# Kernel tuning notes

Measured on AMD Instinct MI355X. Metric: run time of the kernel, lower is better.

The kernel has to match this reference:

```python
import jax, jax.numpy as jnp
import numpy as np

N = 100000      # nodes (categories_nums[0])
E = 1600000     # edges
FEAT = 16       # features_num
HID = 32        # hidden
IDE = 16        # id_embed_size
EMB = 8         # embed_size
CAT_MAX = 1000  # categorical vocab (categories_nums[1:])
K = 3           # TAGConv hops (sparse=False)
NC = 2          # num_class
IN_DIM = IDE + 2 * EMB + HID  # 64 -> TAGConv input
EPS = 1e-5


def layer_norm(x, g, b):
    m = jnp.mean(x, axis=-1, keepdims=True)
    v = jnp.mean((x - m) ** 2, axis=-1, keepdims=True)
    return (x - m) * jax.lax.rsqrt(v + EPS) * g + b


def setup_inputs() -> dict:
    key = jax.random.key(0)
    ks = jax.random.split(key, 20)
    s = 0.05
    return {
        "x": jax.random.normal(ks[0], (N, FEAT), jnp.float32),
        "edge_index": jax.random.randint(ks[1], (2, E), 0, N, jnp.int64),
        "edge_weight": jax.random.uniform(ks[2], (E,), jnp.float32),
        "categories_value": jax.random.randint(ks[3], (N, 3), 0, CAT_MAX, jnp.int64),
        "id_table": jax.random.normal(ks[4], (N, IDE), jnp.float32) * s,
        "lin0_id_W": jax.random.normal(ks[5], (IDE, IDE), jnp.float32) * s,
        "lin0_id_b": jnp.zeros((IDE,), jnp.float32),
        "emb1": jax.random.normal(ks[6], (CAT_MAX, EMB), jnp.float32) * s,
        "emb2": jax.random.normal(ks[7], (CAT_MAX, EMB), jnp.float32) * s,
        "lin0_emb_W": jax.random.normal(ks[8], (2 * EMB, 2 * EMB), jnp.float32) * s,
        "lin0_emb_b": jnp.zeros((2 * EMB,), jnp.float32),
        "lin0_W": jax.random.normal(ks[9], (FEAT, HID), jnp.float32) * s,
        "lin0_b": jnp.zeros((HID,), jnp.float32),
        "ln0_g": jnp.ones((IN_DIM,), jnp.float32),
        "ln0_b": jnp.zeros((IN_DIM,), jnp.float32),
        "tag_W": jax.random.normal(ks[10], (K + 1, IN_DIM, HID), jnp.float32) * s,
        "tag_b": jnp.zeros((HID,), jnp.float32),
        "ln1_g": jnp.ones((HID,), jnp.float32),
        "ln1_b": jnp.zeros((HID,), jnp.float32),
        "lin1_W": jax.random.normal(ks[11], (HID, NC), jnp.float32) * s,
        "lin1_b": jnp.zeros((NC,), jnp.float32),
    }


def reference(x, edge_index, edge_weight, categories_value, id_table, lin0_id_W,
              lin0_id_b, emb1, emb2, lin0_emb_W, lin0_emb_b, lin0_W, lin0_b,
              ln0_g, ln0_b, tag_W, tag_b, ln1_g, ln1_b, lin1_W, lin1_b):
    # eval mode: dropouts are identity
    h = jax.nn.elu(x @ lin0_W + lin0_b)                       # [N, HID]
    ide = id_table[categories_value[:, 0]]                    # [N, IDE]
    ide = jax.nn.elu(ide @ lin0_id_W + lin0_id_b)
    er = jnp.concatenate([emb1[categories_value[:, 1]],
                          emb2[categories_value[:, 2]]], axis=1)  # [N, 2*EMB]
    er = jax.nn.elu(er @ lin0_emb_W + lin0_emb_b)
    feat = jnp.concatenate([ide, h, er], axis=1)              # [N, IN_DIM]
    feat = layer_norm(feat, ln0_g, ln0_b)

    # TAGConv: gcn_norm without self-loops, K-hop propagation
    row, col = edge_index[0], edge_index[1]                   # source -> target
    deg = jax.ops.segment_sum(edge_weight, col, num_segments=N)
    dis = jnp.where(deg > 0, deg ** -0.5, 0.0)
    norm = dis[row] * edge_weight * dis[col]                  # [E]

    out = feat @ tag_W[0]                                     # [N, HID]
    xk = feat
    for k in range(1, K + 1):
        xk = jax.ops.segment_sum(xk[row] * norm[:, None], col, num_segments=N)
        out = out + xk @ tag_W[k]
    out = out + tag_b

    out = jax.nn.relu(out)
    out = layer_norm(out, ln1_g, ln1_b)
    out = out @ lin1_W + lin1_b                               # [N, NC]
    return jax.nn.log_softmax(out, axis=-1)
```

## Files before the change

### kernel.cpp

```cpp
#include <hip/hip_runtime.h>
#include <hip/hip_bf16.h>

typedef unsigned short u16;
typedef unsigned int   u32;
typedef unsigned long long u64;
typedef u32 u32x2 __attribute__((ext_vector_type(2)));
typedef u32 u32x4 __attribute__((ext_vector_type(4)));

#define FIX_SCALE 16777216.0f
#define FIX_INV   (1.0f / 16777216.0f)
#define CNT_SHIFT 40
#define DEG_MASK  ((1ULL << CNT_SHIFT) - 1)

__device__ __forceinline__ float b2f(u16 u) { return __uint_as_float(((u32)u) << 16); }
__device__ __forceinline__ u16 f2b(float f) {
    u32 u = __float_as_uint(f);
    return (u16)((u + 0x7FFFu + ((u >> 16) & 1u)) >> 16);
}
__device__ __forceinline__ float elu(float v) { return v > 0.f ? v : expm1f(v); }
__device__ __forceinline__ float ldf(const void* p, size_t i, int f32) {
    return f32 ? ((const float*)p)[i] : b2f(((const u16*)p)[i]);
}
__device__ __forceinline__ float plo(u32 a) { return __uint_as_float(a << 16); }
__device__ __forceinline__ float phi(u32 a) { return __uint_as_float(a & 0xFFFF0000u); }

__global__ void k_flags(const u32* __restrict__ gw, const int* __restrict__ ei,
                        const int* __restrict__ cat, int* __restrict__ flags) {
    if (threadIdx.x == 0 && blockIdx.x == 0) {
        flags[0] = (gw[0] == 0x3F800000u) ? 1 : 0;
        flags[1] = ((ei[1]  | ei[3]  | ei[5]  | ei[7])  == 0) ? 2 : 1;
        flags[2] = ((cat[1] | cat[3] | cat[5] | cat[7]) == 0) ? 2 : 1;
    }
}

__global__ __launch_bounds__(256) void k_feathist(
    const void* __restrict__ x, const int* __restrict__ cat,
    const void* __restrict__ id_table, const void* __restrict__ W_id, const void* __restrict__ b_id,
    const void* __restrict__ emb1, const void* __restrict__ emb2,
    const void* __restrict__ W_emb, const void* __restrict__ b_emb,
    const void* __restrict__ W0, const void* __restrict__ b0,
    const void* __restrict__ g0, const void* __restrict__ bb0,
    u32* __restrict__ feat,
    const int* __restrict__ ei, const void* __restrict__ ew,
    u64* __restrict__ packed, u16* __restrict__ rank,
    const int* __restrict__ flags, int N, int E, int nbN)
{
    __shared__ float sW0[512];
    __shared__ float sb0[32];
    __shared__ float sWid[256];
    __shared__ float sbid[16];
    __shared__ float sWe[256];
    __shared__ float sbe[16];
    __shared__ float sg[64], sb[64];
    int tid = threadIdx.x;
    int f32 = flags[0], s = flags[1], cs = flags[2];

    int e0 = blockIdx.x * 512 + tid;
    int e1 = e0 + 256;
    u64 old0 = 0, old1 = 0;
    bool h0 = (e0 < E), h1 = (e1 < E);
    const int* colp = ei + (size_t)E * s;
    if (h0) {
        int cdst = colp[(size_t)e0 * s];
        float w = ldf(ew, e0, f32);
        old0 = atomicAdd(&packed[cdst], (1ULL << CNT_SHIFT) | (u64)(w * FIX_SCALE + 0.5f));
    }
    if (h1) {
        int cdst = colp[(size_t)e1 * s];
        float w = ldf(ew, e1, f32);
        old1 = atomicAdd(&packed[cdst], (1ULL << CNT_SHIFT) | (u64)(w * FIX_SCALE + 0.5f));
    }

    if (blockIdx.x < nbN) {
        for (int i = tid; i < 512; i += 256) sW0[i] = ldf(W0, i, f32);
        if (tid < 32) sb0[tid] = ldf(b0, tid, f32);
        sWid[tid] = ldf(W_id, tid, f32);
        if (tid < 16) sbid[tid] = ldf(b_id, tid, f32);
        sWe[tid] = ldf(W_emb, tid, f32);
        if (tid < 16) sbe[tid] = ldf(b_emb, tid, f32);
        if (tid < 64) { sg[tid] = ldf(g0, tid, f32); sb[tid] = ldf(bb0, tid, f32); }
        __syncthreads();

        int i = blockIdx.x * 256 + tid;
        if (i < N) {
            size_t cb = (size_t)i * 3 * cs;
            int c0 = cat[cb], c1 = cat[cb + cs], c2 = cat[cb + 2 * cs];
            float f[64];
            {
                float t[16];
                #pragma unroll
                for (int q = 0; q < 16; q++) t[q] = ldf(id_table, (size_t)c0 * 16 + q, f32);
                #pragma unroll
                for (int j = 0; j < 16; j++) {
                    float a = sbid[j];
                    #pragma unroll
                    for (int ff = 0; ff < 16; ff++) a += t[ff] * sWid[ff * 16 + j];
                    f[j] = elu(a);
                }
            }
            {
                float t[16];
                #pragma unroll
                for (int q = 0; q < 16; q++) t[q] = ldf(x, (size_t)i * 16 + q, f32);
                #pragma unroll
                for (int j = 0; j < 32; j++) {
                    float a = sb0[j];
                    #pragma unroll
                    for (int ff = 0; ff < 16; ff++) a += t[ff] * sW0[ff * 32 + j];
                    f[16 + j] = elu(a);
                }
            }
            {
                float t[16];
                #pragma unroll
                for (int q = 0; q < 8; q++) t[q] = ldf(emb1, (size_t)c1 * 8 + q, f32);
                #pragma unroll
                for (int q = 0; q < 8; q++) t[8 + q] = ldf(emb2, (size_t)c2 * 8 + q, f32);
                #pragma unroll
                for (int j = 0; j < 16; j++) {
                    float a = sbe[j];
                    #pragma unroll
                    for (int ff = 0; ff < 16; ff++) a += t[ff] * sWe[ff * 16 + j];
                    f[48 + j] = elu(a);
                }
            }
            float m = 0.f;
            #pragma unroll
            for (int d = 0; d < 64; d++) m += f[d];
            m *= (1.f / 64.f);
            float var = 0.f;
            #pragma unroll
            for (int d = 0; d < 64; d++) { float df = f[d] - m; var += df * df; }
            var *= (1.f / 64.f);
            float rs = rsqrtf(var + 1e-5f);
            #pragma unroll
            for (int d = 0; d < 64; d++) f[d] = (f[d] - m) * rs * sg[d] + sb[d];

            u32* fp = feat + (size_t)i * 32;
            #pragma unroll
            for (int q = 0; q < 32; q++) fp[q] = ((u32)f2b(f[2 * q + 1]) << 16) | f2b(f[2 * q]);
        }
    }
    if (h0) rank[e0] = (u16)(old0 >> CNT_SHIFT);
    if (h1) rank[e1] = (u16)(old1 >> CNT_SHIFT);
}

__global__ __launch_bounds__(256) void k_zproj(
    const u32* __restrict__ feat, const void* __restrict__ tagW,
    float* __restrict__ oacc, u32* __restrict__ z1, u32* __restrict__ z2, u32* __restrict__ z3,
    const int* __restrict__ flags, int N)
{
    __shared__ float sT[4 * 2056];
    int tid = threadIdx.x;
    int f32 = flags[0];
    for (int i = tid; i < 8192; i += 256) {
        int k = i >> 11, r = i & 2047;
        sT[k * 2056 + r] = ldf(tagW, i, f32);
    }
    __syncthreads();

    int nblk = blockIdx.x * 32 + (tid >> 3);
    if (nblk >= N) return;
    int sub = tid & 7, kk = sub >> 1, h = sub & 1;

    const u32x4* fp4 = (const u32x4*)(feat + (size_t)nblk * 32);
    float f[64];
    #pragma unroll
    for (int q = 0; q < 8; q++) {
        u32x4 a = fp4[q];
        f[8 * q + 0] = plo(a.x); f[8 * q + 1] = phi(a.x);
        f[8 * q + 2] = plo(a.y); f[8 * q + 3] = phi(a.y);
        f[8 * q + 4] = plo(a.z); f[8 * q + 5] = phi(a.z);
        f[8 * q + 6] = plo(a.w); f[8 * q + 7] = phi(a.w);
    }

    float o[16];
    #pragma unroll
    for (int j = 0; j < 16; j++) o[j] = 0.f;
    const float* T = sT + kk * 2056 + h * 16;
    #pragma unroll 4
    for (int d = 0; d < 64; d++) {
        float fd = f[d];
        #pragma unroll
        for (int j = 0; j < 16; j++) o[j] += fd * T[d * 32 + j];
    }

    if (kk == 0) {
        float4* op = (float4*)(oacc + (size_t)nblk * 32 + h * 16);
        #pragma unroll
        for (int q = 0; q < 4; q++) op[q] = make_float4(o[4 * q], o[4 * q + 1], o[4 * q + 2], o[4 * q + 3]);
    } else {
        u32* zp = ((kk == 1) ? z1 : (kk == 2) ? z2 : z3) + (size_t)nblk * 16 + h * 8;
        #pragma unroll
        for (int jj = 0; jj < 8; jj++) zp[jj] = ((u32)f2b(o[2 * jj + 1]) << 16) | f2b(o[2 * jj]);
    }
}

__global__ __launch_bounds__(256) void k_scan1(const u64* __restrict__ packed, int* __restrict__ ebuf,
                                               int* __restrict__ bsum, float* __restrict__ dis, int N)
{
    __shared__ int sdat[256];
    int tid = threadIdx.x;
    int i = blockIdx.x * 256 + tid;
    u64 pv = (i < N) ? packed[i] : 0ULL;
    int v = (int)(pv >> CNT_SHIFT);
    sdat[tid] = v;
    __syncthreads();
    for (int off = 1; off < 256; off <<= 1) {
        int t = (tid >= off) ? sdat[tid - off] : 0;
        __syncthreads();
        sdat[tid] += t;
        __syncthreads();
    }
    if (i < N) {
        ebuf[i] = sdat[tid] - v;
        u64 db = pv & DEG_MASK;
        dis[i] = db ? rsqrtf((float)db * FIX_INV) : 0.f;
    }
    if (tid == 255) bsum[blockIdx.x] = sdat[255];
}

__global__ __launch_bounds__(512) void k_scan2(const int* __restrict__ bsum, int* __restrict__ boff, int NB)
{
    __shared__ int sdat[512];
    __shared__ int scarry;
    int tid = threadIdx.x;
    if (tid == 0) scarry = 0;
    __syncthreads();
    for (int base = 0; base < NB; base += 512) {
        int i = base + tid;
        int v = (i < NB) ? bsum[i] : 0;
        sdat[tid] = v;
        __syncthreads();
        for (int off = 1; off < 512; off <<= 1) {
            int t = (tid >= off) ? sdat[tid - off] : 0;
            __syncthreads();
            sdat[tid] += t;
            __syncthreads();
        }
        if (i < NB) boff[i] = scarry + sdat[tid] - v;
        __syncthreads();
        if (tid == 0) scarry += sdat[511];
        __syncthreads();
    }
}

__global__ __launch_bounds__(256) void k_scan3(const int* __restrict__ ebuf, const int* __restrict__ boff,
                                               int* __restrict__ rowptr, int N, int E)
{
    int i = blockIdx.x * 256 + threadIdx.x;
    if (i >= N) return;
    rowptr[i] = boff[blockIdx.x] + ebuf[i];
    if (i == N - 1) rowptr[N] = E;
}

__global__ __launch_bounds__(256) void k_scatter(const int* __restrict__ ei, const void* __restrict__ ew,
                                                 const float* __restrict__ dis, const u16* __restrict__ rank,
                                                 const int* __restrict__ rowptr, int2* __restrict__ csr,
                                                 const int* __restrict__ flags, int E)
{
    int f32 = flags[0], s = flags[1];
    const int* row = ei;
    const int* col = ei + (size_t)E * s;
    int e = blockIdx.x * 256 + threadIdx.x;
    if (e >= E) return;
    int r = row[(size_t)e * s], c = col[(size_t)e * s];
    float nrm = dis[r] * ldf(ew, e, f32) * dis[c];
    csr[rowptr[c] + (int)rank[e]] = make_int2(r, __float_as_int(nrm));
}

template<int ADD>
__global__ __launch_bounds__(256) void k_ahop(
    const u32* __restrict__ zin, const u32* __restrict__ zadd, u32* __restrict__ uout,
    const int* __restrict__ rowptr, const int2* __restrict__ csr, int N)
{
    int tid = threadIdx.x;
    int node = blockIdx.x * 4 + (tid >> 6);
    if (node >= N) return;
    int lane = tid & 63;
    int o = (lane >> 3) & 7;
    int c = lane & 7;
    int start = rowptr[node], end = rowptr[node + 1];

    const u32x2* fin2 = (const u32x2*)zin;
    float v0 = 0.f, v1 = 0.f, v2 = 0.f, v3 = 0.f;
    int e = start;
    for (; e + 16 <= end; e += 16) {
        int2 ma = csr[e + o];
        int2 mb = csr[e + 8 + o];
        u32x2 aa = fin2[(size_t)(u32)ma.x * 8 + c];
        u32x2 ab = fin2[(size_t)(u32)mb.x * 8 + c];
        float wa = __int_as_float(ma.y), wb = __int_as_float(mb.y);
        v0 += plo(aa.x) * wa; v1 += phi(aa.x) * wa; v2 += plo(aa.y) * wa; v3 += phi(aa.y) * wa;
        v0 += plo(ab.x) * wb; v1 += phi(ab.x) * wb; v2 += plo(ab.y) * wb; v3 += phi(ab.y) * wb;
    }
    for (; e < end; e += 8) {
        int ee = e + o;
        int2 m = (ee < end) ? csr[ee] : make_int2(0, 0);
        u32x2 a = fin2[(size_t)(u32)m.x * 8 + c];
        float w = __int_as_float(m.y);
        v0 += plo(a.x) * w; v1 += phi(a.x) * w; v2 += plo(a.y) * w; v3 += phi(a.y) * w;
    }
    v0 += __shfl_xor(v0, 8);  v1 += __shfl_xor(v1, 8);  v2 += __shfl_xor(v2, 8);  v3 += __shfl_xor(v3, 8);
    v0 += __shfl_xor(v0, 16); v1 += __shfl_xor(v1, 16); v2 += __shfl_xor(v2, 16); v3 += __shfl_xor(v3, 16);
    v0 += __shfl_xor(v0, 32); v1 += __shfl_xor(v1, 32); v2 += __shfl_xor(v2, 32); v3 += __shfl_xor(v3, 32);

    if (lane < 8) {
        if (ADD) {
            u32x2 z = ((const u32x2*)zadd)[(size_t)node * 8 + lane];
            v0 += plo(z.x); v1 += phi(z.x); v2 += plo(z.y); v3 += phi(z.y);
        }
        u32x2 pw;
        pw.x = ((u32)f2b(v1) << 16) | f2b(v0);
        pw.y = ((u32)f2b(v3) << 16) | f2b(v2);
        ((u32x2*)uout)[(size_t)node * 8 + lane] = pw;
    }
}

__global__ __launch_bounds__(256) void k_head(
    const float* __restrict__ oacc, const u32* __restrict__ t1,
    const void* __restrict__ tag_b,
    const void* __restrict__ g1, const void* __restrict__ b1,
    const void* __restrict__ W1, const void* __restrict__ bb1,
    void* __restrict__ out, const int* __restrict__ flags, int N)
{
    __shared__ float stb[32], sg[32], sbb[32], sW1[64], sb1v[2];
    int tid = threadIdx.x;
    int f32 = flags[0];
    if (tid < 32) { stb[tid] = ldf(tag_b, tid, f32); sg[tid] = ldf(g1, tid, f32); sbb[tid] = ldf(b1, tid, f32); }
    if (tid < 64) sW1[tid] = ldf(W1, tid, f32);
    if (tid < 2) sb1v[tid] = ldf(bb1, tid, f32);
    __syncthreads();

    int i = blockIdx.x * 256 + tid;
    if (i >= N) return;

    float acc[32];
    const float4* oa4 = (const float4*)(oacc + (size_t)i * 32);
    #pragma unroll
    for (int q = 0; q < 8; q++) {
        float4 t = oa4[q];
        acc[4 * q] = t.x; acc[4 * q + 1] = t.y; acc[4 * q + 2] = t.z; acc[4 * q + 3] = t.w;
    }
    const u32x2* tp = (const u32x2*)t1 + (size_t)i * 8;
    #pragma unroll
    for (int q = 0; q < 8; q++) {
        u32x2 z = tp[q];
        acc[4 * q]     += plo(z.x); acc[4 * q + 1] += phi(z.x);
        acc[4 * q + 2] += plo(z.y); acc[4 * q + 3] += phi(z.y);
    }
    float o[32]; float m = 0.f;
    #pragma unroll
    for (int j = 0; j < 32; j++) { float t = acc[j] + stb[j]; t = t > 0.f ? t : 0.f; o[j] = t; m += t; }
    m *= (1.f / 32.f);
    float var = 0.f;
    #pragma unroll
    for (int j = 0; j < 32; j++) { float d = o[j] - m; var += d * d; }
    var *= (1.f / 32.f);
    float rs = rsqrtf(var + 1e-5f);
    float z0 = sb1v[0], z1 = sb1v[1];
    #pragma unroll
    for (int j = 0; j < 32; j++) {
        float t = (o[j] - m) * rs * sg[j] + sbb[j];
        z0 += t * sW1[2 * j];
        z1 += t * sW1[2 * j + 1];
    }
    float mx = fmaxf(z0, z1);
    float l = mx + logf(expf(z0 - mx) + expf(z1 - mx));
    if (f32) {
        ((float*)out)[(size_t)i * 2]     = z0 - l;
        ((float*)out)[(size_t)i * 2 + 1] = z1 - l;
    } else {
        *((u32*)((u16*)out + (size_t)i * 2)) = ((u32)f2b(z1 - l) << 16) | f2b(z0 - l);
    }
}

extern "C" void kernel_launch(void* const* d_in, const int* in_sizes, int n_in,
                              void* d_out, int out_size, void* d_ws, size_t ws_size,
                              hipStream_t stream)
{
    const void* x        = d_in[0];
    const int*  ei       = (const int*)d_in[1];
    const void* ew       = d_in[2];
    const int*  cat      = (const int*)d_in[3];
    const void* id_table = d_in[4];
    const void* W_id     = d_in[5];
    const void* b_id     = d_in[6];
    const void* emb1     = d_in[7];
    const void* emb2     = d_in[8];
    const void* W_emb    = d_in[9];
    const void* b_emb    = d_in[10];
    const void* W0       = d_in[11];
    const void* b0       = d_in[12];
    const void* g0       = d_in[13];
    const void* bb0      = d_in[14];
    const void* tagW     = d_in[15];
    const void* tag_b    = d_in[16];
    const void* g1       = d_in[17];
    const void* b1       = d_in[18];
    const void* W1       = d_in[19];
    const void* bb1      = d_in[20];

    int N = in_sizes[0] / 16;
    int E = in_sizes[2];
    int nb = (N + 255) / 256;
    int eb = (E + 255) / 256;
    int eb2 = (E + 511) / 512;
    int zb = (N + 31) / 32;

    char* ws = (char*)d_ws;
    size_t off = 0;
    int*   flags  = (int*)(ws + off);   off += 256;
    float* oacc   = (float*)(ws + off); off += (size_t)N * 32 * 4;
    u32*   feat   = (u32*)(ws + off);   off += (size_t)N * 32 * 4;
    u32*   z1     = (u32*)(ws + off);   off += (size_t)N * 16 * 4;
    u32*   z2     = (u32*)(ws + off);   off += (size_t)N * 16 * 4;
    u32*   z3     = (u32*)(ws + off);   off += (size_t)N * 16 * 4;
    u32*   u2     = (u32*)(ws + off);   off += (size_t)N * 16 * 4;
    int2*  csr    = (int2*)(ws + off);  off += (size_t)E * 8;
    int*   rowptr = (int*)(ws + off);   off += ((size_t)N + 1) * 4;
    off = (off + 255) & ~(size_t)255;
    u16*   rank   = (u16*)(ws + off);   off += (size_t)E * 2;
    off = (off + 255) & ~(size_t)255;
    u64*   packed = (u64*)(ws + off);   off += (size_t)N * 8;
    int*   ebuf   = (int*)(ws + off);   off += (size_t)N * 4;
    float* dis    = (float*)(ws + off); off += (size_t)N * 4;
    int*   bsum   = (int*)(ws + off);   off += (size_t)nb * 4;
    int*   boff   = (int*)(ws + off);   off += (size_t)nb * 4;

    hipMemsetAsync(packed, 0, (size_t)N * 8, stream);
    k_flags<<<1, 64, 0, stream>>>((const u32*)g0, ei, cat, flags);

    k_feathist<<<eb2, 256, 0, stream>>>(x, cat, id_table, W_id, b_id, emb1, emb2, W_emb, b_emb,
                                        W0, b0, g0, bb0, feat,
                                        ei, ew, packed, rank, flags, N, E, nb);
    k_zproj<<<zb, 256, 0, stream>>>(feat, tagW, oacc, z1, z2, z3, flags, N);

    k_scan1<<<nb, 256, 0, stream>>>(packed, ebuf, bsum, dis, N);
    k_scan2<<<1, 512, 0, stream>>>(bsum, boff, nb);
    k_scan3<<<nb, 256, 0, stream>>>(ebuf, boff, rowptr, N, E);
    k_scatter<<<eb, 256, 0, stream>>>(ei, ew, dis, rank, rowptr, csr, flags, E);

    int hb = (N + 3) / 4;
    k_ahop<1><<<hb, 256, 0, stream>>>(z3, z2, u2, rowptr, csr, N);
    k_ahop<1><<<hb, 256, 0, stream>>>(u2, z1, z3, rowptr, csr, N);
    k_ahop<0><<<hb, 256, 0, stream>>>(z3, z1, z2, rowptr, csr, N);
    k_head<<<nb, 256, 0, stream>>>(oacc, z2, tag_b, g1, b1, W1, bb1, d_out, flags, N);
}
```

Baseline: 455.4 us.

## Restructure TAG projection kernel to keep weights in registers and stage features in LDS

```diff
diff --git a/kernel.cpp b/kernel.cpp
--- a/kernel.cpp
+++ b/kernel.cpp
@@ -150,49 +150,62 @@
     float* __restrict__ oacc, u32* __restrict__ z1, u32* __restrict__ z2, u32* __restrict__ z3,
     const int* __restrict__ flags, int N)
 {
-    __shared__ float sT[4 * 2056];
+    __shared__ u32x4 sF[512];
     int tid = threadIdx.x;
     int f32 = flags[0];
-    for (int i = tid; i < 8192; i += 256) {
-        int k = i >> 11, r = i & 2047;
-        sT[k * 2056 + r] = ldf(tagW, i, f32);
-    }
+    int wid = tid >> 6;
+    int lane = tid & 63;
+    int j = lane & 31;
+    int dh = lane >> 5;
+
+    float w[32];
+    {
+        size_t base = (size_t)wid * 2048 + (size_t)dh * 1024 + j;
+        #pragma unroll
+        for (int dd = 0; dd < 32; dd++) w[dd] = ldf(tagW, base + (size_t)dd * 32, f32);
+    }
+
+    int nb0 = blockIdx.x * 64;
+    int nv = N - nb0; if (nv > 64) nv = 64; if (nv < 0) nv = 0;
+    for (int i = tid; i < nv * 8; i += 256)
+        sF[i] = ((const u32x4*)feat)[(size_t)nb0 * 8 + i];
     __syncthreads();
 
-    int nblk = blockIdx.x * 32 + (tid >> 3);
-    if (nblk >= N) return;
-    int sub = tid & 7, kk = sub >> 1, h = sub & 1;
-
-    const u32x4* fp4 = (const u32x4*)(feat + (size_t)nblk * 32);
-    float f[64];
-    #pragma unroll
-    for (int q = 0; q < 8; q++) {
-        u32x4 a = fp4[q];
-        f[8 * q + 0] = plo(a.x); f[8 * q + 1] = phi(a.x);
-        f[8 * q + 2] = plo(a.y); f[8 * q + 3] = phi(a.y);
-        f[8 * q + 4] = plo(a.z); f[8 * q + 5] = phi(a.z);
-        f[8 * q + 6] = plo(a.w); f[8 * q + 7] = phi(a.w);
-    }
-
-    float o[16];
-    #pragma unroll
-    for (int j = 0; j < 16; j++) o[j] = 0.f;
-    const float* T = sT + kk * 2056 + h * 16;
-    #pragma unroll 4
-    for (int d = 0; d < 64; d++) {
-        float fd = f[d];
-        #pragma unroll
-        for (int j = 0; j < 16; j++) o[j] += fd * T[d * 32 + j];
-    }
-
-    if (kk == 0) {
-        float4* op = (float4*)(oacc + (size_t)nblk * 32 + h * 16);
-        #pragma unroll
-        for (int q = 0; q < 4; q++) op[q] = make_float4(o[4 * q], o[4 * q + 1], o[4 * q + 2], o[4 * q + 3]);
-    } else {
-        u32* zp = ((kk == 1) ? z1 : (kk == 2) ? z2 : z3) + (size_t)nblk * 16 + h * 8;
-        #pragma unroll
-        for (int jj = 0; jj < 8; jj++) zp[jj] = ((u32)f2b(o[2 * jj + 1]) << 16) | f2b(o[2 * jj]);
+    u32* zp = (wid == 1) ? z1 : (wid == 2) ? z2 : z3;
+
+    #pragma unroll 2
+    for (int n = 0; n < nv; n++) {
+        const u32x4* fp = sF + n * 8 + dh * 4;
+        u32x4 r0 = fp[0], r1 = fp[1], r2 = fp[2], r3 = fp[3];
+        float za = 0.f, zb = 0.f;
+        za += plo(r0.x) * w[0];  zb += phi(r0.x) * w[1];
+        za += plo(r0.y) * w[2];  zb += phi(r0.y) * w[3];
+        za += plo(r0.z) * w[4];  zb += phi(r0.z) * w[5];
+        za += plo(r0.w) * w[6];  zb += phi(r0.w) * w[7];
+        za += plo(r1.x) * w[8];  zb += phi(r1.x) * w[9];
+        za += plo(r1.y) * w[10]; zb += phi(r1.y) * w[11];
+        za += plo(r1.z) * w[12]; zb += phi(r1.z) * w[13];
+        za += plo(r1.w) * w[14]; zb += phi(r1.w) * w[15];
+        za += plo(r2.x) * w[16]; zb += phi(r2.x) * w[17];
+        za += plo(r2.y) * w[18]; zb += phi(r2.y) * w[19];
+        za += plo(r2.z) * w[20]; zb += phi(r2.z) * w[21];
+        za += plo(r2.w) * w[22]; zb += phi(r2.w) * w[23];
+        za += plo(r3.x) * w[24]; zb += phi(r3.x) * w[25];
+        za += plo(r3.y) * w[26]; zb += phi(r3.y) * w[27];
+        za += plo(r3.z) * w[28]; zb += phi(r3.z) * w[29];
+        za += plo(r3.w) * w[30]; zb += phi(r3.w) * w[31];
+        float z = za + zb;
+        z += __shfl_xor(z, 32);
+
+        int gnode = nb0 + n;
+        if (wid == 0) {
+            if (lane < 32) oacc[(size_t)gnode * 32 + j] = z;
+        } else {
+            float zlo = __shfl(z, 2 * lane);
+            float zhi = __shfl(z, 2 * lane + 1);
+            if (lane < 16)
+                zp[(size_t)gnode * 16 + lane] = ((u32)f2b(zhi) << 16) | f2b(zlo);
+        }
     }
 }
 
@@ -406,7 +419,7 @@
     int nb = (N + 255) / 256;
     int eb = (E + 255) / 256;
     int eb2 = (E + 511) / 512;
-    int zb = (N + 31) / 32;
+    int zb = (N + 63) / 64;
 
     char* ws = (char*)d_ws;
     size_t off = 0;
```

Measured after the change: 386.4 us. 1.18x faster.
